# Performance work log

Measured on AMD Instinct MI355X. Metric: run time of the kernel, lower is better.

## Reference

```python
import jax, jax.numpy as jnp
import numpy as np

N_NODES = 100000


def setup_inputs() -> dict:
    key = jax.random.key(0)
    k1, k2, k3, k4 = jax.random.split(key, 4)
    N, E, D = N_NODES, 1200000, 64
    graph_embedding = jax.random.normal(k1, (N, D), dtype=jnp.float32)
    e_feat = jax.random.normal(k2, (E,), dtype=jnp.float32)
    src_idx = jax.random.randint(k3, (E,), 0, N, dtype=jnp.int32)
    dst_idx = jax.random.randint(k4, (E,), 0, N, dtype=jnp.int32)
    return {"graph_embedding": graph_embedding, "e_feat": e_feat,
            "src_idx": src_idx, "dst_idx": dst_idx}


def reference(graph_embedding, e_feat, src_idx, dst_idx):
    # message per edge: concat(src node feature [E,D], edge feature [E,1]) -> [E,D+1]
    e = e_feat.reshape(-1, 1).astype(jnp.float32)          # [E,1]
    msg = jnp.concatenate([graph_embedding[src_idx], e], axis=1)  # [E,D+1]
    # scatter-sum messages to destination nodes -> [N,D+1]
    res = jax.ops.segment_sum(msg, dst_idx, num_segments=N_NODES)
    return res
```

## Files before the change

kernel.cpp:

```cpp
#include <hip/hip_runtime.h>
#include <hip/hip_fp16.h>


#define NB_SHIFT 6
#define BNODES   64
#define SRC_BITS 17
#define SRC_MASK ((1 << SRC_BITS) - 1)
#define BIN_S    4096
#define BIN_T    512
#define MAXNB    2048

__global__ void conv_half_kernel(const float* __restrict__ g, __half* __restrict__ h, int n) {
    int i = (blockIdx.x * blockDim.x + threadIdx.x) * 8;
    if (i + 7 < n) {
        float4 a = *(const float4*)(g + i);
        float4 b = *(const float4*)(g + i + 4);
        __half2 h0 = __floats2half2_rn(a.x, a.y);
        __half2 h1 = __floats2half2_rn(a.z, a.w);
        __half2 h2 = __floats2half2_rn(b.x, b.y);
        __half2 h3 = __floats2half2_rn(b.z, b.w);
        int4 o;
        o.x = *(int*)&h0; o.y = *(int*)&h1; o.z = *(int*)&h2; o.w = *(int*)&h3;
        *(int4*)(h + i) = o;
    } else {
        for (int k = i; k < n; ++k) h[k] = __float2half(g[k]);
    }
}

__global__ __launch_bounds__(BIN_T) void minihist_kernel(const int* __restrict__ dst,
                                                         int* __restrict__ counts,
                                                         int E, int NB) {
    __shared__ int cnt[MAXNB];
    int t = threadIdx.x;
    for (int i = t; i < MAXNB; i += BIN_T) cnt[i] = 0;
    __syncthreads();
    int e0 = blockIdx.x * BIN_S + t * 8;
    if (e0 + 7 < E) {
        int4 a = *(const int4*)(dst + e0);
        int4 b = *(const int4*)(dst + e0 + 4);
        atomicAdd(&cnt[a.x >> NB_SHIFT], 1);
        atomicAdd(&cnt[a.y >> NB_SHIFT], 1);
        atomicAdd(&cnt[a.z >> NB_SHIFT], 1);
        atomicAdd(&cnt[a.w >> NB_SHIFT], 1);
        atomicAdd(&cnt[b.x >> NB_SHIFT], 1);
        atomicAdd(&cnt[b.y >> NB_SHIFT], 1);
        atomicAdd(&cnt[b.z >> NB_SHIFT], 1);
        atomicAdd(&cnt[b.w >> NB_SHIFT], 1);
    } else {
        for (int k = e0; k < E; ++k) atomicAdd(&cnt[dst[k] >> NB_SHIFT], 1);
    }
    __syncthreads();
    for (int i = t; i < NB; i += BIN_T)
        if (cnt[i]) atomicAdd(&counts[i], cnt[i]);
}

__global__ void scan_kernel(const int* __restrict__ counts,
                            int* __restrict__ goff, int* __restrict__ gcur,
                            int NB) {
    __shared__ int sh[1024];
    int t = threadIdx.x;
    int c0 = (2 * t     < NB) ? counts[2 * t]     : 0;
    int c1 = (2 * t + 1 < NB) ? counts[2 * t + 1] : 0;
    int s  = c0 + c1;
    sh[t] = s;
    __syncthreads();
    for (int o = 1; o < 1024; o <<= 1) {
        int u = (t >= o) ? sh[t - o] : 0;
        __syncthreads();
        sh[t] += u;
        __syncthreads();
    }
    int ex = sh[t] - s;
    if (2 * t < NB)     { goff[2 * t]     = ex;      gcur[2 * t]     = ex;      }
    if (2 * t + 1 < NB) { goff[2 * t + 1] = ex + c0; gcur[2 * t + 1] = ex + c0; }
    if (t == 1023) goff[NB] = sh[1023];
}

__global__ __launch_bounds__(BIN_T) void bin_kernel(const int* __restrict__ src,
                                                    const float* __restrict__ ef,
                                                    const int* __restrict__ dst,
                                                    int* __restrict__ gcur,
                                                    int2* __restrict__ gpay, int E) {
    __shared__ int cnt[MAXNB];
    __shared__ int lbase[MAXNB];
    __shared__ int pscan[BIN_T];
    __shared__ int2 stage[BIN_S];
    __shared__ unsigned short sbuck[BIN_S];

    int t = threadIdx.x;
    for (int i = t; i < MAXNB; i += BIN_T) cnt[i] = 0;
    __syncthreads();

    int e0 = blockIdx.x * BIN_S + t * 8;
    int dv[8], sv[8], bk[8], rk[8];
    float ev[8];

    if (e0 + 7 < E) {
        *(int4*)&dv[0]   = *(const int4*)(dst + e0);
        *(int4*)&dv[4]   = *(const int4*)(dst + e0 + 4);
        *(int4*)&sv[0]   = *(const int4*)(src + e0);
        *(int4*)&sv[4]   = *(const int4*)(src + e0 + 4);
        *(float4*)&ev[0] = *(const float4*)(ef + e0);
        *(float4*)&ev[4] = *(const float4*)(ef + e0 + 4);
#pragma unroll
        for (int k = 0; k < 8; ++k) {
            bk[k] = dv[k] >> NB_SHIFT;
            rk[k] = atomicAdd(&cnt[bk[k]], 1);
        }
    } else {
#pragma unroll
        for (int k = 0; k < 8; ++k) {
            if (e0 + k < E) {
                dv[k] = dst[e0 + k];
                sv[k] = src[e0 + k];
                ev[k] = ef[e0 + k];
                bk[k] = dv[k] >> NB_SHIFT;
                rk[k] = atomicAdd(&cnt[bk[k]], 1);
            } else {
                bk[k] = -1;
            }
        }
    }
    __syncthreads();

    int c0 = cnt[4 * t], c1 = cnt[4 * t + 1], c2 = cnt[4 * t + 2], c3 = cnt[4 * t + 3];
    int ts = c0 + c1 + c2 + c3;
    pscan[t] = ts;
    __syncthreads();
    for (int o = 1; o < BIN_T; o <<= 1) {
        int u = (t >= o) ? pscan[t - o] : 0;
        __syncthreads();
        pscan[t] += u;
        __syncthreads();
    }
    int ex = pscan[t] - ts;
    lbase[4 * t]     = ex;
    lbase[4 * t + 1] = ex + c0;
    lbase[4 * t + 2] = ex + c0 + c1;
    lbase[4 * t + 3] = ex + c0 + c1 + c2;
    __syncthreads();

#pragma unroll
    for (int k = 0; k < 8; ++k) {
        if (bk[k] >= 0) {
            int pos = lbase[bk[k]] + rk[k];
            stage[pos] = make_int2(((dv[k] & (BNODES - 1)) << SRC_BITS) | sv[k],
                                   __float_as_int(ev[k]));
            sbuck[pos] = (unsigned short)bk[k];
        }
    }
    for (int i = t; i < MAXNB; i += BIN_T) {
        int c = cnt[i];
        cnt[i] = (c ? atomicAdd(&gcur[i], c) : 0) - lbase[i];
    }
    __syncthreads();

    int s_total = min(BIN_S, E - blockIdx.x * BIN_S);
    for (int i = t; i < s_total; i += BIN_T) {
        int b = sbuck[i];
        gpay[cnt[b] + i] = stage[i];
    }
}

__global__ __launch_bounds__(256) void bsort_kernel(const int2* __restrict__ gpay,
                                                    const int* __restrict__ goff,
                                                    int2* __restrict__ gpay2,
                                                    int* __restrict__ noff,
                                                    int N, int E) {
    __shared__ int cnt[BNODES];
    __shared__ int sbuf[BNODES];
    __shared__ int cur[BNODES];

    const int t  = threadIdx.x;
    const int b  = blockIdx.x;
    const int lo = goff[b];
    const int hi = goff[b + 1];

    if (t < BNODES) cnt[t] = 0;
    __syncthreads();

    for (int i = lo + t; i < hi; i += 256)
        atomicAdd(&cnt[gpay[i].x >> SRC_BITS], 1);
    __syncthreads();

    int v = (t < BNODES) ? cnt[t] : 0;
    if (t < BNODES) sbuf[t] = v;
    __syncthreads();
    for (int o = 1; o < BNODES; o <<= 1) {
        int u = (t < BNODES && t >= o) ? sbuf[t - o] : 0;
        __syncthreads();
        if (t < BNODES) sbuf[t] += u;
        __syncthreads();
    }
    if (t < BNODES) {
        int base = lo + sbuf[t] - v;
        cur[t] = base;
        int node = b * BNODES + t;
        if (node <= N) noff[node] = base;
    }
    if (b == 0 && t == 0) noff[N] = E;
    __syncthreads();

    for (int i = lo + t; i < hi; i += 256) {
        int2 p = gpay[i];
        int pos = atomicAdd(&cur[p.x >> SRC_BITS], 1);
        gpay2[pos] = p;
    }
}

__global__ void gather_h_kernel(const __half* __restrict__ hg,
                                const int2* __restrict__ pack,
                                const int* __restrict__ noff,
                                float* __restrict__ out, int N) {
    int wid  = (blockIdx.x * blockDim.x + threadIdx.x) >> 6;
    int lane = threadIdx.x & 63;
    if (wid >= N) return;

    int beg = noff[wid];
    int end = noff[wid + 1];

    float a0 = 0.f, a1 = 0.f, a2 = 0.f, a3 = 0.f;
    float a4 = 0.f, a5 = 0.f, a6 = 0.f, a7 = 0.f;
    float ea = 0.f, eb = 0.f;
    int j = beg;
    for (; j + 7 < end; j += 8) {
        int2 v0 = pack[j];     int2 v1 = pack[j + 1];
        int2 v2 = pack[j + 2]; int2 v3 = pack[j + 3];
        int2 v4 = pack[j + 4]; int2 v5 = pack[j + 5];
        int2 v6 = pack[j + 6]; int2 v7 = pack[j + 7];
        a0 += __half2float(hg[(size_t)(v0.x & SRC_MASK) * 64 + lane]);
        a1 += __half2float(hg[(size_t)(v1.x & SRC_MASK) * 64 + lane]);
        a2 += __half2float(hg[(size_t)(v2.x & SRC_MASK) * 64 + lane]);
        a3 += __half2float(hg[(size_t)(v3.x & SRC_MASK) * 64 + lane]);
        a4 += __half2float(hg[(size_t)(v4.x & SRC_MASK) * 64 + lane]);
        a5 += __half2float(hg[(size_t)(v5.x & SRC_MASK) * 64 + lane]);
        a6 += __half2float(hg[(size_t)(v6.x & SRC_MASK) * 64 + lane]);
        a7 += __half2float(hg[(size_t)(v7.x & SRC_MASK) * 64 + lane]);
        ea += __int_as_float(v0.y) + __int_as_float(v1.y) +
              __int_as_float(v2.y) + __int_as_float(v3.y);
        eb += __int_as_float(v4.y) + __int_as_float(v5.y) +
              __int_as_float(v6.y) + __int_as_float(v7.y);
    }
    for (; j + 3 < end; j += 4) {
        int2 v0 = pack[j];     int2 v1 = pack[j + 1];
        int2 v2 = pack[j + 2]; int2 v3 = pack[j + 3];
        a0 += __half2float(hg[(size_t)(v0.x & SRC_MASK) * 64 + lane]);
        a1 += __half2float(hg[(size_t)(v1.x & SRC_MASK) * 64 + lane]);
        a2 += __half2float(hg[(size_t)(v2.x & SRC_MASK) * 64 + lane]);
        a3 += __half2float(hg[(size_t)(v3.x & SRC_MASK) * 64 + lane]);
        ea += __int_as_float(v0.y) + __int_as_float(v1.y) +
              __int_as_float(v2.y) + __int_as_float(v3.y);
    }
    for (; j < end; ++j) {
        int2 v = pack[j];
        a0 += __half2float(hg[(size_t)(v.x & SRC_MASK) * 64 + lane]);
        ea += __int_as_float(v.y);
    }
    out[(size_t)wid * 65 + lane] = ((a0 + a1) + (a2 + a3)) + ((a4 + a5) + (a6 + a7));
    if (lane == 0) out[(size_t)wid * 65 + 64] = ea + eb;
}


__global__ void atomic_fallback_kernel(const float* __restrict__ gemb,
                                       const float* __restrict__ efeat,
                                       const int* __restrict__ src,
                                       const int* __restrict__ dst,
                                       float* __restrict__ out, int E) {
    int eidx = blockIdx.x * 4 + (threadIdx.x >> 6);
    int lane = threadIdx.x & 63;
    if (eidx >= E) return;
    int s = src[eidx];
    int d = dst[eidx];
    float v = gemb[(size_t)s * 64 + lane];
    atomicAdd(&out[(size_t)d * 65 + lane], v);
    if (lane == 0) atomicAdd(&out[(size_t)d * 65 + 64], efeat[eidx]);
}


extern "C" void kernel_launch(void* const* d_in, const int* in_sizes, int n_in,
                              void* d_out, int out_size, void* d_ws, size_t ws_size,
                              hipStream_t stream) {
    const float* gemb  = (const float*)d_in[0];
    const float* efeat = (const float*)d_in[1];
    const int*   src   = (const int*)d_in[2];
    const int*   dst   = (const int*)d_in[3];
    float*       out   = (float*)d_out;

    const int N  = in_sizes[0] / 64;
    const int E  = in_sizes[1];
    const int NB = (N + BNODES - 1) >> NB_SHIFT;

    auto aln = [](size_t x) { return (x + 15) & ~(size_t)15; };
    size_t off_counts = 0;
    size_t off_goff   = off_counts + aln((size_t)NB * 4);
    size_t off_gcur   = off_goff   + aln((size_t)(NB + 1) * 4);
    size_t off_noff   = off_gcur   + aln((size_t)NB * 4);
    size_t off_gpay   = off_noff   + aln((size_t)(N + 1) * 4);
    size_t off_gpay2  = off_gpay   + aln((size_t)E * 8);
    size_t off_hg     = off_gpay2  + aln((size_t)E * 8);
    size_t needed     = off_hg     + (size_t)N * 64 * 2;

    if (N > (1 << SRC_BITS) || NB > MAXNB || ws_size < needed) {
        hipMemsetAsync(d_out, 0, (size_t)out_size * sizeof(float), stream);
        int blocks = (E + 3) / 4;
        atomic_fallback_kernel<<<blocks, 256, 0, stream>>>(gemb, efeat, src, dst, out, E);
        return;
    }

    char*   ws     = (char*)d_ws;
    int*    counts = (int*)(ws + off_counts);
    int*    goff   = (int*)(ws + off_goff);
    int*    gcur   = (int*)(ws + off_gcur);
    int*    noff   = (int*)(ws + off_noff);
    int2*   gpay   = (int2*)(ws + off_gpay);
    int2*   gpay2  = (int2*)(ws + off_gpay2);
    __half* hg     = (__half*)(ws + off_hg);

    hipMemsetAsync(counts, 0, (size_t)NB * 4, stream);

    int n_emb    = N * 64;
    int c_blocks = ((n_emb + 7) / 8 + 255) / 256;
    conv_half_kernel<<<c_blocks, 256, 0, stream>>>(gemb, hg, n_emb);

    int e_blocks = (E + BIN_S - 1) / BIN_S;
    minihist_kernel<<<e_blocks, BIN_T, 0, stream>>>(dst, counts, E, NB);
    scan_kernel<<<1, 1024, 0, stream>>>(counts, goff, gcur, NB);
    bin_kernel<<<e_blocks, BIN_T, 0, stream>>>(src, efeat, dst, gcur, gpay, E);
    bsort_kernel<<<NB, 256, 0, stream>>>(gpay, goff, gpay2, noff, N, E);

    int g_blocks = (N + 3) / 4;
    gather_h_kernel<<<g_blocks, 256, 0, stream>>>(hg, gpay2, noff, out, N);
}
```

Measured before the change: 114.2 us.

## Fuse conversion with histogram, move edge-feature sums into bucket sort, use wave scans

The fp32-to-fp16 conversion and the destination histogram now run as one launch, with blocks split by index, which removes one kernel launch and lets the two independent jobs overlap. The bucket sort now writes only 4-byte source indices instead of 8-byte pairs. It also accumulates the edge-feature column per node with shared-memory float atomics and writes it directly, so the gather kernel reads half as much index data. Block-wide scans in the bin and sort kernels are replaced by wavefront shuffle scans that need fewer barriers. Float atomics make the edge-feature sum order nondeterministic.

```diff
diff --git a/kernel.cpp b/kernel.cpp
--- a/kernel.cpp
+++ b/kernel.cpp
@@ -10,31 +10,37 @@
 #define BIN_T    512
 #define MAXNB    2048
 
-__global__ void conv_half_kernel(const float* __restrict__ g, __half* __restrict__ h, int n) {
-    int i = (blockIdx.x * blockDim.x + threadIdx.x) * 8;
-    if (i + 7 < n) {
-        float4 a = *(const float4*)(g + i);
-        float4 b = *(const float4*)(g + i + 4);
-        __half2 h0 = __floats2half2_rn(a.x, a.y);
-        __half2 h1 = __floats2half2_rn(a.z, a.w);
-        __half2 h2 = __floats2half2_rn(b.x, b.y);
-        __half2 h3 = __floats2half2_rn(b.z, b.w);
-        int4 o;
-        o.x = *(int*)&h0; o.y = *(int*)&h1; o.z = *(int*)&h2; o.w = *(int*)&h3;
-        *(int4*)(h + i) = o;
-    } else {
-        for (int k = i; k < n; ++k) h[k] = __float2half(g[k]);
-    }
-}
-
-__global__ __launch_bounds__(BIN_T) void minihist_kernel(const int* __restrict__ dst,
+__global__ __launch_bounds__(BIN_T) void convhist_kernel(const float* __restrict__ g,
+                                                         __half* __restrict__ h,
+                                                         int n_emb, int c_blocks,
+                                                         const int* __restrict__ dst,
                                                          int* __restrict__ counts,
                                                          int E, int NB) {
     __shared__ int cnt[MAXNB];
     int t = threadIdx.x;
+
+    if (blockIdx.x < c_blocks) {
+        int i = (blockIdx.x * BIN_T + t) * 8;
+        if (i + 7 < n_emb) {
+            float4 a = *(const float4*)(g + i);
+            float4 b = *(const float4*)(g + i + 4);
+            __half2 h0 = __floats2half2_rn(a.x, a.y);
+            __half2 h1 = __floats2half2_rn(a.z, a.w);
+            __half2 h2 = __floats2half2_rn(b.x, b.y);
+            __half2 h3 = __floats2half2_rn(b.z, b.w);
+            int4 o;
+            o.x = *(int*)&h0; o.y = *(int*)&h1; o.z = *(int*)&h2; o.w = *(int*)&h3;
+            *(int4*)(h + i) = o;
+        } else {
+            for (int k = i; k < n_emb; ++k) h[k] = __float2half(g[k]);
+        }
+        return;
+    }
+
+    int hb = blockIdx.x - c_blocks;
     for (int i = t; i < MAXNB; i += BIN_T) cnt[i] = 0;
     __syncthreads();
-    int e0 = blockIdx.x * BIN_S + t * 8;
+    int e0 = hb * BIN_S + t * 8;
     if (e0 + 7 < E) {
         int4 a = *(const int4*)(dst + e0);
         int4 b = *(const int4*)(dst + e0 + 4);
@@ -83,11 +89,15 @@
                                                     int2* __restrict__ gpay, int E) {
     __shared__ int cnt[MAXNB];
     __shared__ int lbase[MAXNB];
-    __shared__ int pscan[BIN_T];
+    __shared__ int wsum[8];
+    __shared__ int wbase[8];
     __shared__ int2 stage[BIN_S];
     __shared__ unsigned short sbuck[BIN_S];
 
-    int t = threadIdx.x;
+    const int t    = threadIdx.x;
+    const int lane = t & 63;
+    const int wv   = t >> 6;
+
     for (int i = t; i < MAXNB; i += BIN_T) cnt[i] = 0;
     __syncthreads();
 
@@ -125,15 +135,26 @@
 
     int c0 = cnt[4 * t], c1 = cnt[4 * t + 1], c2 = cnt[4 * t + 2], c3 = cnt[4 * t + 3];
     int ts = c0 + c1 + c2 + c3;
-    pscan[t] = ts;
-    __syncthreads();
-    for (int o = 1; o < BIN_T; o <<= 1) {
-        int u = (t >= o) ? pscan[t - o] : 0;
-        __syncthreads();
-        pscan[t] += u;
-        __syncthreads();
-    }
-    int ex = pscan[t] - ts;
+    int incl = ts;
+#pragma unroll
+    for (int o = 1; o < 64; o <<= 1) {
+        int u = __shfl_up(incl, o);
+        if (lane >= o) incl += u;
+    }
+    if (lane == 63) wsum[wv] = incl;
+    __syncthreads();
+    if (t < 8) {
+        int v = wsum[t];
+        int inc = v;
+#pragma unroll
+        for (int o = 1; o < 8; o <<= 1) {
+            int u = __shfl_up(inc, o);
+            if (t >= o) inc += u;
+        }
+        wbase[t] = inc - v;
+    }
+    __syncthreads();
+    int ex = wbase[wv] + (incl - ts);
     lbase[4 * t]     = ex;
     lbase[4 * t + 1] = ex + c0;
     lbase[4 * t + 2] = ex + c0 + c1;
@@ -164,36 +185,35 @@
 
 __global__ __launch_bounds__(256) void bsort_kernel(const int2* __restrict__ gpay,
                                                     const int* __restrict__ goff,
-                                                    int2* __restrict__ gpay2,
+                                                    int* __restrict__ gsrc2,
                                                     int* __restrict__ noff,
+                                                    float* __restrict__ out,
                                                     int N, int E) {
-    __shared__ int cnt[BNODES];
-    __shared__ int sbuf[BNODES];
-    __shared__ int cur[BNODES];
+    __shared__ int   cnt[BNODES];
+    __shared__ int   cur[BNODES];
+    __shared__ float esum[BNODES];
 
     const int t  = threadIdx.x;
     const int b  = blockIdx.x;
     const int lo = goff[b];
     const int hi = goff[b + 1];
 
-    if (t < BNODES) cnt[t] = 0;
+    if (t < BNODES) { cnt[t] = 0; esum[t] = 0.f; }
     __syncthreads();
 
     for (int i = lo + t; i < hi; i += 256)
         atomicAdd(&cnt[gpay[i].x >> SRC_BITS], 1);
     __syncthreads();
 
-    int v = (t < BNODES) ? cnt[t] : 0;
-    if (t < BNODES) sbuf[t] = v;
-    __syncthreads();
-    for (int o = 1; o < BNODES; o <<= 1) {
-        int u = (t < BNODES && t >= o) ? sbuf[t - o] : 0;
-        __syncthreads();
-        if (t < BNODES) sbuf[t] += u;
-        __syncthreads();
-    }
-    if (t < BNODES) {
-        int base = lo + sbuf[t] - v;
+    if (t < 64) {
+        int v = cnt[t];
+        int inc = v;
+#pragma unroll
+        for (int o = 1; o < 64; o <<= 1) {
+            int u = __shfl_up(inc, o);
+            if (t >= o) inc += u;
+        }
+        int base = lo + inc - v;
         cur[t] = base;
         int node = b * BNODES + t;
         if (node <= N) noff[node] = base;
@@ -203,13 +223,21 @@
 
     for (int i = lo + t; i < hi; i += 256) {
         int2 p = gpay[i];
-        int pos = atomicAdd(&cur[p.x >> SRC_BITS], 1);
-        gpay2[pos] = p;
+        int  r = p.x >> SRC_BITS;
+        int pos = atomicAdd(&cur[r], 1);
+        gsrc2[pos] = p.x & SRC_MASK;
+        atomicAdd(&esum[r], __int_as_float(p.y));
+    }
+    __syncthreads();
+
+    if (t < 64) {
+        int node = b * BNODES + t;
+        if (node < N) out[(size_t)node * 65 + 64] = esum[t];
     }
 }
 
 __global__ void gather_h_kernel(const __half* __restrict__ hg,
-                                const int2* __restrict__ pack,
+                                const int* __restrict__ gs,
                                 const int* __restrict__ noff,
                                 float* __restrict__ out, int N) {
     int wid  = (blockIdx.x * blockDim.x + threadIdx.x) >> 6;
@@ -221,43 +249,33 @@
 
     float a0 = 0.f, a1 = 0.f, a2 = 0.f, a3 = 0.f;
     float a4 = 0.f, a5 = 0.f, a6 = 0.f, a7 = 0.f;
-    float ea = 0.f, eb = 0.f;
     int j = beg;
     for (; j + 7 < end; j += 8) {
-        int2 v0 = pack[j];     int2 v1 = pack[j + 1];
-        int2 v2 = pack[j + 2]; int2 v3 = pack[j + 3];
-        int2 v4 = pack[j + 4]; int2 v5 = pack[j + 5];
-        int2 v6 = pack[j + 6]; int2 v7 = pack[j + 7];
-        a0 += __half2float(hg[(size_t)(v0.x & SRC_MASK) * 64 + lane]);
-        a1 += __half2float(hg[(size_t)(v1.x & SRC_MASK) * 64 + lane]);
-        a2 += __half2float(hg[(size_t)(v2.x & SRC_MASK) * 64 + lane]);
-        a3 += __half2float(hg[(size_t)(v3.x & SRC_MASK) * 64 + lane]);
-        a4 += __half2float(hg[(size_t)(v4.x & SRC_MASK) * 64 + lane]);
-        a5 += __half2float(hg[(size_t)(v5.x & SRC_MASK) * 64 + lane]);
-        a6 += __half2float(hg[(size_t)(v6.x & SRC_MASK) * 64 + lane]);
-        a7 += __half2float(hg[(size_t)(v7.x & SRC_MASK) * 64 + lane]);
-        ea += __int_as_float(v0.y) + __int_as_float(v1.y) +
-              __int_as_float(v2.y) + __int_as_float(v3.y);
-        eb += __int_as_float(v4.y) + __int_as_float(v5.y) +
-              __int_as_float(v6.y) + __int_as_float(v7.y);
+        int s0 = gs[j];     int s1 = gs[j + 1];
+        int s2 = gs[j + 2]; int s3 = gs[j + 3];
+        int s4 = gs[j + 4]; int s5 = gs[j + 5];
+        int s6 = gs[j + 6]; int s7 = gs[j + 7];
+        a0 += __half2float(hg[(size_t)s0 * 64 + lane]);
+        a1 += __half2float(hg[(size_t)s1 * 64 + lane]);
+        a2 += __half2float(hg[(size_t)s2 * 64 + lane]);
+        a3 += __half2float(hg[(size_t)s3 * 64 + lane]);
+        a4 += __half2float(hg[(size_t)s4 * 64 + lane]);
+        a5 += __half2float(hg[(size_t)s5 * 64 + lane]);
+        a6 += __half2float(hg[(size_t)s6 * 64 + lane]);
+        a7 += __half2float(hg[(size_t)s7 * 64 + lane]);
     }
     for (; j + 3 < end; j += 4) {
-        int2 v0 = pack[j];     int2 v1 = pack[j + 1];
-        int2 v2 = pack[j + 2]; int2 v3 = pack[j + 3];
-        a0 += __half2float(hg[(size_t)(v0.x & SRC_MASK) * 64 + lane]);
-        a1 += __half2float(hg[(size_t)(v1.x & SRC_MASK) * 64 + lane]);
-        a2 += __half2float(hg[(size_t)(v2.x & SRC_MASK) * 64 + lane]);
-        a3 += __half2float(hg[(size_t)(v3.x & SRC_MASK) * 64 + lane]);
-        ea += __int_as_float(v0.y) + __int_as_float(v1.y) +
-              __int_as_float(v2.y) + __int_as_float(v3.y);
+        int s0 = gs[j];     int s1 = gs[j + 1];
+        int s2 = gs[j + 2]; int s3 = gs[j + 3];
+        a0 += __half2float(hg[(size_t)s0 * 64 + lane]);
+        a1 += __half2float(hg[(size_t)s1 * 64 + lane]);
+        a2 += __half2float(hg[(size_t)s2 * 64 + lane]);
+        a3 += __half2float(hg[(size_t)s3 * 64 + lane]);
     }
     for (; j < end; ++j) {
-        int2 v = pack[j];
-        a0 += __half2float(hg[(size_t)(v.x & SRC_MASK) * 64 + lane]);
-        ea += __int_as_float(v.y);
+        a0 += __half2float(hg[(size_t)gs[j] * 64 + lane]);
     }
     out[(size_t)wid * 65 + lane] = ((a0 + a1) + (a2 + a3)) + ((a4 + a5) + (a6 + a7));
-    if (lane == 0) out[(size_t)wid * 65 + 64] = ea + eb;
 }
 
 
@@ -296,8 +314,8 @@
     size_t off_gcur   = off_goff   + aln((size_t)(NB + 1) * 4);
     size_t off_noff   = off_gcur   + aln((size_t)NB * 4);
     size_t off_gpay   = off_noff   + aln((size_t)(N + 1) * 4);
-    size_t off_gpay2  = off_gpay   + aln((size_t)E * 8);
-    size_t off_hg     = off_gpay2  + aln((size_t)E * 8);
+    size_t off_gsrc2  = off_gpay   + aln((size_t)E * 8);
+    size_t off_hg     = off_gsrc2  + aln((size_t)E * 4);
     size_t needed     = off_hg     + (size_t)N * 64 * 2;
 
     if (N > (1 << SRC_BITS) || NB > MAXNB || ws_size < needed) {
@@ -313,21 +331,21 @@
     int*    gcur   = (int*)(ws + off_gcur);
     int*    noff   = (int*)(ws + off_noff);
     int2*   gpay   = (int2*)(ws + off_gpay);
-    int2*   gpay2  = (int2*)(ws + off_gpay2);
+    int*    gsrc2  = (int*)(ws + off_gsrc2);
     __half* hg     = (__half*)(ws + off_hg);
 
     hipMemsetAsync(counts, 0, (size_t)NB * 4, stream);
 
     int n_emb    = N * 64;
-    int c_blocks = ((n_emb + 7) / 8 + 255) / 256;
-    conv_half_kernel<<<c_blocks, 256, 0, stream>>>(gemb, hg, n_emb);
-
-    int e_blocks = (E + BIN_S - 1) / BIN_S;
-    minihist_kernel<<<e_blocks, BIN_T, 0, stream>>>(dst, counts, E, NB);
+    int c_blocks = (n_emb + BIN_T * 8 - 1) / (BIN_T * 8);
+    int h_blocks = (E + BIN_S - 1) / BIN_S;
+    convhist_kernel<<<c_blocks + h_blocks, BIN_T, 0, stream>>>(
+        gemb, hg, n_emb, c_blocks, dst, counts, E, NB);
+
     scan_kernel<<<1, 1024, 0, stream>>>(counts, goff, gcur, NB);
-    bin_kernel<<<e_blocks, BIN_T, 0, stream>>>(src, efeat, dst, gcur, gpay, E);
-    bsort_kernel<<<NB, 256, 0, stream>>>(gpay, goff, gpay2, noff, N, E);
+    bin_kernel<<<h_blocks, BIN_T, 0, stream>>>(src, efeat, dst, gcur, gpay, E);
+    bsort_kernel<<<NB, 256, 0, stream>>>(gpay, goff, gsrc2, noff, out, N, E);
 
     int g_blocks = (N + 3) / 4;
-    gather_h_kernel<<<g_blocks, 256, 0, stream>>>(hg, gpay2, noff, out, N);
-}
+    gather_h_kernel<<<g_blocks, 256, 0, stream>>>(hg, gsrc2, noff, out, N);
+}
```

After: 110.1 us. -3.6%, faster.
